# Performance work log

Measured on AMD Instinct MI355X. Metric: run time of the kernel, lower is better.

## Reference

```python
import jax, jax.numpy as jnp
import numpy as np

BN_EPS = 1e-3  # keras BatchNormalization default epsilon


def setup_inputs() -> dict:
    key = jax.random.key(0)
    ks = jax.random.split(key, 8)
    B, F, Df = 256, 64, 256   # batch, num_features, feature_dim
    E, H, D = 8, 256, 256     # num_experts, hidden, expert_dim
    s1 = 1.0 / np.sqrt(Df)
    s2 = 1.0 / np.sqrt(H)
    return {
        "x":  jax.random.normal(ks[0], (B, F, Df), jnp.float32),
        "Wr": jax.random.normal(ks[1], (Df, E), jnp.float32) * s1,
        "br": jnp.zeros((E,), jnp.float32),
        "W1": jax.random.normal(ks[2], (E, Df, H), jnp.float32) * s1,
        "b1": jnp.zeros((E, H), jnp.float32),
        "g1": jnp.ones((E, H), jnp.float32),
        "be1": jnp.zeros((E, H), jnp.float32),
        "m1": jnp.zeros((E, H), jnp.float32),
        "v1": jnp.ones((E, H), jnp.float32),
        "W2": jax.random.normal(ks[3], (E, H, H), jnp.float32) * s2,
        "b2": jnp.zeros((E, H), jnp.float32),
        "g2": jnp.ones((E, H), jnp.float32),
        "be2": jnp.zeros((E, H), jnp.float32),
        "m2": jnp.zeros((E, H), jnp.float32),
        "v2": jnp.ones((E, H), jnp.float32),
        "Wo": jax.random.normal(ks[4], (E, H, D), jnp.float32) * s2,
        "bo": jnp.zeros((E, D), jnp.float32),
    }


def _bn(h, g, b, m, v):
    # inference-mode batch norm with moving stats; params are [E,H], h is [B,F,E,H]
    return g * (h - m) * jax.lax.rsqrt(v + BN_EPS) + b


def reference(x, Wr, br, W1, b1, g1, be1, m1, v1,
              W2, b2, g2, be2, m2, v2, Wo, bo):
    # learned softmax routing: mean over batch -> [F, Df] -> dense -> softmax
    feat = jnp.mean(x, axis=0)                     # [F, Df]
    w = jax.nn.softmax(feat @ Wr + br, axis=-1)    # [F, E]

    # all experts at once: Dense -> BN -> relu, x2, then Dense output
    h = jnp.einsum('bfd,edh->bfeh', x, W1) + b1    # [B, F, E, H]
    h = jax.nn.relu(_bn(h, g1, be1, m1, v1))
    h = jnp.einsum('bfeh,ehk->bfek', h, W2) + b2
    h = jax.nn.relu(_bn(h, g2, be2, m2, v2))
    y = jnp.einsum('bfeh,ehd->bfed', h, Wo) + bo   # [B, F, E, D]

    # weighted combine over experts (routing weights broadcast over batch)
    return jnp.einsum('bfed,fe->bfd', y, w)        # [B, F, D]
```

## Files before the change

### kernel.cpp

```cpp
#include <hip/hip_runtime.h>
#include <hip/hip_bf16.h>
#include <stdint.h>

#define BN_EPS 1e-3f

typedef __bf16 bf16x8 __attribute__((ext_vector_type(8)));
typedef float  f32x16 __attribute__((ext_vector_type(16)));

static constexpr size_t WS_FOLD_OFF = 24ull * 131072ull;
static constexpr size_t WS_WRT_OFF  = WS_FOLD_OFF + 32768ull;
static constexpr size_t WS_WB_OFF   = WS_WRT_OFF + 2048ull;

#define XADDR(fr, tok) (((fr) << 10) + ((((tok) ^ (fr))) << 4))

__global__ __launch_bounds__(256) void fold_kernel(
    const float* __restrict__ b1, const float* __restrict__ g1, const float* __restrict__ be1,
    const float* __restrict__ m1, const float* __restrict__ v1,
    const float* __restrict__ b2, const float* __restrict__ g2, const float* __restrict__ be2,
    const float* __restrict__ m2, const float* __restrict__ v2,
    float* __restrict__ fold) {
  int i = blockIdx.x * 256 + threadIdx.x;
  if (i < 2048) {
    float s1 = g1[i] * rsqrtf(v1[i] + BN_EPS);
    fold[i]        = s1;
    fold[2048 + i] = (b1[i] - m1[i]) * s1 + be1[i];
    float s2 = g2[i] * rsqrtf(v2[i] + BN_EPS);
    fold[4096 + i] = s2;
    fold[6144 + i] = (b2[i] - m2[i]) * s2 + be2[i];
  }
}

__global__ __launch_bounds__(256) void pack_kernel(
    const float* __restrict__ W1, const float* __restrict__ W2, const float* __restrict__ Wo,
    __bf16* __restrict__ pk) {
  __shared__ float sl[16 * 256];
  int bid = blockIdx.x;
  int m = bid >> 4, ks = bid & 15;
  int L = m >> 3, e = m & 7;
  const float* Ws = (L == 0 ? W1 : (L == 1 ? W2 : Wo)) + (size_t)e * 65536 + (size_t)ks * 16 * 256;
  int t = threadIdx.x;
#pragma unroll
  for (int it = 0; it < 4; ++it) {
    int el4 = it * 256 + t;
    float4 v = *reinterpret_cast<const float4*>(Ws + (size_t)el4 * 4);
    *reinterpret_cast<float4*>(&sl[el4 * 4]) = v;
  }
  __syncthreads();
#pragma unroll
  for (int it = 0; it < 2; ++it) {
    int task = it * 256 + t;
    int nb = task >> 6, l = task & 63;
    int colb = nb * 32 + (l & 31);
    int krow = (l >> 5) * 8;
    union { __bf16 h[8]; int4 v; } u;
#pragma unroll
    for (int i = 0; i < 8; ++i) u.h[i] = (__bf16)sl[(krow + i) * 256 + colb];
    size_t off = ((size_t)(m * 8 + nb) * 16 + ks) * 512 + (size_t)l * 8;
    *reinterpret_cast<int4*>(pk + off) = u.v;
  }
}

__global__ __launch_bounds__(256) void route1_kernel(
    const float* __restrict__ x, float* __restrict__ part) {
  int f = blockIdx.x, bq = blockIdx.y, t = threadIdx.x;
  const float* xp = x + (size_t)(bq * 32) * 16384 + f * 256 + t;
  float s = 0.f;
#pragma unroll 4
  for (int bi = 0; bi < 32; ++bi) s += xp[(size_t)bi * 16384];
  part[(size_t)(bq * 64 + f) * 256 + t] = s;
}

__global__ __launch_bounds__(256) void route2_kernel(
    const float* __restrict__ part, const float* __restrict__ Wr, const float* __restrict__ br,
    const float* __restrict__ bo, float* __restrict__ wrt, float* __restrict__ wb) {
  __shared__ float feat[256];
  __shared__ float lg[8];
  __shared__ float wsm[8];
  int f = blockIdx.x, t = threadIdx.x;
  float a = 0.f;
#pragma unroll
  for (int bq = 0; bq < 8; ++bq) a += part[(size_t)(bq * 64 + f) * 256 + t];
  feat[t] = a * (1.0f / 256.0f);
  __syncthreads();
  if (t < 8) {
    float s = br[t];
    for (int d = 0; d < 256; ++d) s += feat[d] * Wr[d * 8 + t];
    lg[t] = s;
  }
  __syncthreads();
  if (t == 0) {
    float mx = lg[0];
#pragma unroll
    for (int e = 1; e < 8; ++e) mx = fmaxf(mx, lg[e]);
    float ex[8]; float sum = 0.f;
#pragma unroll
    for (int e = 0; e < 8; ++e) { ex[e] = expf(lg[e] - mx); sum += ex[e]; }
    float inv = 1.0f / sum;
#pragma unroll
    for (int e = 0; e < 8; ++e) { float v = ex[e] * inv; wsm[e] = v; wrt[f * 8 + e] = v; }
  }
  __syncthreads();
  float o = 0.f;
#pragma unroll
  for (int e = 0; e < 8; ++e) o += wsm[e] * bo[e * 256 + t];
  wb[f * 256 + t] = o;
}

__device__ __forceinline__ void sweep(
    const char* __restrict__ src, const __bf16* __restrict__ pb,
    int l, int l31, int hi, int swap, int zero, f32x16 acc[2]) {
  if (zero) {
#pragma unroll
    for (int mt = 0; mt < 2; ++mt)
#pragma unroll
      for (int r = 0; r < 16; ++r) acc[mt][r] = 0.f;
  }
  bf16x8 b0 = *reinterpret_cast<const bf16x8*>(pb + (size_t)l * 8);
  bf16x8 b1 = *reinterpret_cast<const bf16x8*>(pb + 512 + (size_t)l * 8);
#pragma unroll
  for (int ks = 0; ks < 16; ++ks) {
    bf16x8 bn = (ks < 14) ? *reinterpret_cast<const bf16x8*>(pb + (size_t)(ks + 2) * 512 + (size_t)l * 8) : b0;
    int fr = 2 * ks + hi;
    bf16x8 a0 = *reinterpret_cast<const bf16x8*>(src + XADDR(fr, l31));
    bf16x8 a1 = *reinterpret_cast<const bf16x8*>(src + XADDR(fr, 32 + l31));
    if (swap) {
      acc[0] = __builtin_amdgcn_mfma_f32_32x32x16_bf16(b0, a0, acc[0], 0, 0, 0);
      acc[1] = __builtin_amdgcn_mfma_f32_32x32x16_bf16(b0, a1, acc[1], 0, 0, 0);
    } else {
      acc[0] = __builtin_amdgcn_mfma_f32_32x32x16_bf16(a0, b0, acc[0], 0, 0, 0);
      acc[1] = __builtin_amdgcn_mfma_f32_32x32x16_bf16(a1, b0, acc[1], 0, 0, 0);
    }
    b0 = b1; b1 = bn;
  }
}

__device__ __forceinline__ void epi_store(
    const f32x16 acc[2], const float* __restrict__ sA, const float* __restrict__ cA,
    char* __restrict__ dst, int l31, int hi, int w, float w0, float w1) {
#pragma unroll
  for (int g = 0; g < 4; ++g) {
    float4 s4 = *reinterpret_cast<const float4*>(sA + 8 * g);
    float4 c4 = *reinterpret_cast<const float4*>(cA + 8 * g);
    int fr = w * 4 + g;
#pragma unroll
    for (int mt = 0; mt < 2; ++mt) {
      float wm = (mt == 0) ? w0 : w1;
      union { __bf16 h[4]; uint2 u; } p;
#pragma unroll
      for (int j = 0; j < 4; ++j) {
        float sj = (&s4.x)[j], cj = (&c4.x)[j];
        p.h[j] = (__bf16)(wm * fmaxf(acc[mt][4 * g + j] * sj + cj, 0.f));
      }
      *reinterpret_cast<uint2*>(dst + XADDR(fr, mt * 32 + l31) + hi * 8) = p.u;
    }
  }
}

__global__ __launch_bounds__(512, 4) void moe_kernel(
    const float* __restrict__ x, const __bf16* __restrict__ pk,
    const float* __restrict__ fold, const float* __restrict__ wrt,
    const float* __restrict__ wb, float* __restrict__ out) {
  __shared__ char xb[32768];
  __shared__ char hb[32768];
  __shared__ float wrts[512];
  const int tid = threadIdx.x;
  const int l = tid & 63, w = tid >> 6;
  const int l31 = l & 31, hi = l >> 5;
  const int bid = blockIdx.x;
  const int tile = bid >> 1, eh = bid & 1;

  {
    const float* xg = x + (size_t)tile * 16384;
#pragma unroll
    for (int i = 0; i < 4; ++i) {
      int u = i * 512 + tid;
      int tok = u >> 5, k8 = u & 31;
      const float* src = xg + (size_t)tok * 256 + k8 * 8;
      float4 v0 = *reinterpret_cast<const float4*>(src);
      float4 v1 = *reinterpret_cast<const float4*>(src + 4);
      union { __bf16 h[8]; int4 v; } p;
      p.h[0] = (__bf16)v0.x; p.h[1] = (__bf16)v0.y; p.h[2] = (__bf16)v0.z; p.h[3] = (__bf16)v0.w;
      p.h[4] = (__bf16)v1.x; p.h[5] = (__bf16)v1.y; p.h[6] = (__bf16)v1.z; p.h[7] = (__bf16)v1.w;
      *reinterpret_cast<int4*>(xb + XADDR(k8, tok)) = p.v;
    }
  }
  wrts[tid] = wrt[tid];

  f32x16 outacc[2];
#pragma unroll
  for (int mt = 0; mt < 2; ++mt)
#pragma unroll
    for (int r = 0; r < 16; ++r) outacc[mt][r] = 0.f;

  __syncthreads();

  f32x16 acc[2];
#pragma unroll 1
  for (int ep = 0; ep < 4; ++ep) {
    const int e = eh * 4 + ep;
    sweep(xb, pk + (size_t)((0 * 8 + e) * 8 + w) * 8192, l, l31, hi, 1, 1, acc);
    __syncthreads();
    epi_store(acc, fold + 0 * 4096 + e * 256 + w * 32 + 4 * hi,
              fold + 0 * 4096 + 2048 + e * 256 + w * 32 + 4 * hi, hb, l31, hi, w, 1.f, 1.f);
    __syncthreads();
    sweep(hb, pk + (size_t)((1 * 8 + e) * 8 + w) * 8192, l, l31, hi, 1, 1, acc);
    __syncthreads();
    {
      float w0 = wrts[l31 * 8 + e];
      float w1 = wrts[(32 + l31) * 8 + e];
      epi_store(acc, fold + 1 * 4096 + e * 256 + w * 32 + 4 * hi,
                fold + 1 * 4096 + 2048 + e * 256 + w * 32 + 4 * hi, hb, l31, hi, w, w0, w1);
    }
    __syncthreads();
    sweep(hb, pk + (size_t)((2 * 8 + e) * 8 + w) * 8192, l, l31, hi, 0, 0, outacc);
  }

  float* og = out + (size_t)tile * 16384;
  const int col = w * 32 + l31;
#pragma unroll
  for (int mt = 0; mt < 2; ++mt) {
#pragma unroll
    for (int r = 0; r < 16; ++r) {
      int row = mt * 32 + 4 * hi + (r & 3) + 8 * (r >> 2);
      float v = outacc[mt][r];
      if (eh == 0) v += wb[row * 256 + col];
      unsafeAtomicAdd(og + row * 256 + col, v);
    }
  }
}

extern "C" void kernel_launch(void* const* d_in, const int* in_sizes, int n_in,
                              void* d_out, int out_size, void* d_ws, size_t ws_size,
                              hipStream_t stream) {
  const float* x   = (const float*)d_in[0];
  const float* Wr  = (const float*)d_in[1];
  const float* br  = (const float*)d_in[2];
  const float* W1  = (const float*)d_in[3];
  const float* b1  = (const float*)d_in[4];
  const float* g1  = (const float*)d_in[5];
  const float* be1 = (const float*)d_in[6];
  const float* m1  = (const float*)d_in[7];
  const float* v1  = (const float*)d_in[8];
  const float* W2  = (const float*)d_in[9];
  const float* b2  = (const float*)d_in[10];
  const float* g2  = (const float*)d_in[11];
  const float* be2 = (const float*)d_in[12];
  const float* m2  = (const float*)d_in[13];
  const float* v2  = (const float*)d_in[14];
  const float* Wo  = (const float*)d_in[15];
  const float* bo  = (const float*)d_in[16];
  float* out = (float*)d_out;

  __bf16* pk  = (__bf16*)d_ws;
  float* part = (float*)d_ws;
  float* fold = (float*)((char*)d_ws + WS_FOLD_OFF);
  float* wrt  = (float*)((char*)d_ws + WS_WRT_OFF);
  float* wb   = (float*)((char*)d_ws + WS_WB_OFF);

  hipMemsetAsync(out, 0, (size_t)out_size * sizeof(float), stream);
  hipLaunchKernelGGL(route1_kernel, dim3(64, 8), dim3(256), 0, stream, x, part);
  hipLaunchKernelGGL(route2_kernel, dim3(64), dim3(256), 0, stream, part, Wr, br, bo, wrt, wb);
  hipLaunchKernelGGL(fold_kernel, dim3(8), dim3(256), 0, stream,
                     b1, g1, be1, m1, v1, b2, g2, be2, m2, v2, fold);
  hipLaunchKernelGGL(pack_kernel, dim3(384), dim3(256), 0, stream, W1, W2, Wo, pk);
  hipLaunchKernelGGL(moe_kernel, dim3(512), dim3(512), 0, stream, x, pk, fold, wrt, wb, out);
}
```

Baseline: 123.8 us.

## Enlarge MoE block tile to 128 tokens with 2x2 warp MFMA tiling

```diff
diff --git a/kernel.cpp b/kernel.cpp
--- a/kernel.cpp
+++ b/kernel.cpp
@@ -11,7 +11,7 @@
 static constexpr size_t WS_WRT_OFF  = WS_FOLD_OFF + 32768ull;
 static constexpr size_t WS_WB_OFF   = WS_WRT_OFF + 2048ull;
 
-#define XADDR(fr, tok) (((fr) << 10) + ((((tok) ^ (fr))) << 4))
+#define XADDR(fr, tok) (((fr) << 11) + ((((tok) ^ ((fr) & 31))) << 4))
 
 __global__ __launch_bounds__(256) void fold_kernel(
     const float* __restrict__ b1, const float* __restrict__ g1, const float* __restrict__ be1,
@@ -106,73 +106,82 @@
   wb[f * 256 + t] = o;
 }
 
-__device__ __forceinline__ void sweep(
+__device__ __forceinline__ void sweep128(
     const char* __restrict__ src, const __bf16* __restrict__ pb,
-    int l, int l31, int hi, int swap, int zero, f32x16 acc[2]) {
+    int l, int l31, int hi, int mtg, int swap, int zero, f32x16 acc[2][2]) {
   if (zero) {
 #pragma unroll
-    for (int mt = 0; mt < 2; ++mt)
-#pragma unroll
-      for (int r = 0; r < 16; ++r) acc[mt][r] = 0.f;
-  }
-  bf16x8 b0 = *reinterpret_cast<const bf16x8*>(pb + (size_t)l * 8);
-  bf16x8 b1 = *reinterpret_cast<const bf16x8*>(pb + 512 + (size_t)l * 8);
+    for (int nbi = 0; nbi < 2; ++nbi)
+#pragma unroll
+      for (int mt = 0; mt < 2; ++mt)
+#pragma unroll
+        for (int r = 0; r < 16; ++r) acc[nbi][mt][r] = 0.f;
+  }
 #pragma unroll
   for (int ks = 0; ks < 16; ++ks) {
-    bf16x8 bn = (ks < 14) ? *reinterpret_cast<const bf16x8*>(pb + (size_t)(ks + 2) * 512 + (size_t)l * 8) : b0;
+    bf16x8 b0 = *reinterpret_cast<const bf16x8*>(pb + (size_t)ks * 512 + (size_t)l * 8);
+    bf16x8 b1 = *reinterpret_cast<const bf16x8*>(pb + 8192 + (size_t)ks * 512 + (size_t)l * 8);
     int fr = 2 * ks + hi;
-    bf16x8 a0 = *reinterpret_cast<const bf16x8*>(src + XADDR(fr, l31));
-    bf16x8 a1 = *reinterpret_cast<const bf16x8*>(src + XADDR(fr, 32 + l31));
+    bf16x8 a0 = *reinterpret_cast<const bf16x8*>(src + XADDR(fr, mtg * 64 + l31));
+    bf16x8 a1 = *reinterpret_cast<const bf16x8*>(src + XADDR(fr, mtg * 64 + 32 + l31));
     if (swap) {
-      acc[0] = __builtin_amdgcn_mfma_f32_32x32x16_bf16(b0, a0, acc[0], 0, 0, 0);
-      acc[1] = __builtin_amdgcn_mfma_f32_32x32x16_bf16(b0, a1, acc[1], 0, 0, 0);
+      acc[0][0] = __builtin_amdgcn_mfma_f32_32x32x16_bf16(b0, a0, acc[0][0], 0, 0, 0);
+      acc[0][1] = __builtin_amdgcn_mfma_f32_32x32x16_bf16(b0, a1, acc[0][1], 0, 0, 0);
+      acc[1][0] = __builtin_amdgcn_mfma_f32_32x32x16_bf16(b1, a0, acc[1][0], 0, 0, 0);
+      acc[1][1] = __builtin_amdgcn_mfma_f32_32x32x16_bf16(b1, a1, acc[1][1], 0, 0, 0);
     } else {
-      acc[0] = __builtin_amdgcn_mfma_f32_32x32x16_bf16(a0, b0, acc[0], 0, 0, 0);
-      acc[1] = __builtin_amdgcn_mfma_f32_32x32x16_bf16(a1, b0, acc[1], 0, 0, 0);
-    }
-    b0 = b1; b1 = bn;
+      acc[0][0] = __builtin_amdgcn_mfma_f32_32x32x16_bf16(a0, b0, acc[0][0], 0, 0, 0);
+      acc[0][1] = __builtin_amdgcn_mfma_f32_32x32x16_bf16(a1, b0, acc[0][1], 0, 0, 0);
+      acc[1][0] = __builtin_amdgcn_mfma_f32_32x32x16_bf16(a0, b1, acc[1][0], 0, 0, 0);
+      acc[1][1] = __builtin_amdgcn_mfma_f32_32x32x16_bf16(a1, b1, acc[1][1], 0, 0, 0);
+    }
   }
 }
 
 __device__ __forceinline__ void epi_store(
-    const f32x16 acc[2], const float* __restrict__ sA, const float* __restrict__ cA,
-    char* __restrict__ dst, int l31, int hi, int w, float w0, float w1) {
-#pragma unroll
-  for (int g = 0; g < 4; ++g) {
-    float4 s4 = *reinterpret_cast<const float4*>(sA + 8 * g);
-    float4 c4 = *reinterpret_cast<const float4*>(cA + 8 * g);
-    int fr = w * 4 + g;
-#pragma unroll
-    for (int mt = 0; mt < 2; ++mt) {
-      float wm = (mt == 0) ? w0 : w1;
-      union { __bf16 h[4]; uint2 u; } p;
-#pragma unroll
-      for (int j = 0; j < 4; ++j) {
-        float sj = (&s4.x)[j], cj = (&c4.x)[j];
-        p.h[j] = (__bf16)(wm * fmaxf(acc[mt][4 * g + j] * sj + cj, 0.f));
+    const f32x16 acc[2][2], const float* __restrict__ sA, const float* __restrict__ cA,
+    char* __restrict__ dst, int l31, int hi, int mtg, int wn, float w0, float w1) {
+#pragma unroll
+  for (int nbi = 0; nbi < 2; ++nbi) {
+#pragma unroll
+    for (int g = 0; g < 4; ++g) {
+      float4 s4 = *reinterpret_cast<const float4*>(sA + nbi * 32 + 8 * g);
+      float4 c4 = *reinterpret_cast<const float4*>(cA + nbi * 32 + 8 * g);
+      int fr = (wn * 2 + nbi) * 4 + g;
+#pragma unroll
+      for (int mt = 0; mt < 2; ++mt) {
+        float wm = (mt == 0) ? w0 : w1;
+        union { __bf16 h[4]; uint2 u; } p;
+#pragma unroll
+        for (int j = 0; j < 4; ++j) {
+          float sj = (&s4.x)[j], cj = (&c4.x)[j];
+          p.h[j] = (__bf16)(wm * fmaxf(acc[nbi][mt][4 * g + j] * sj + cj, 0.f));
+        }
+        int tok = mtg * 64 + mt * 32 + l31;
+        *reinterpret_cast<uint2*>(dst + XADDR(fr, tok) + hi * 8) = p.u;
       }
-      *reinterpret_cast<uint2*>(dst + XADDR(fr, mt * 32 + l31) + hi * 8) = p.u;
-    }
-  }
-}
-
-__global__ __launch_bounds__(512, 4) void moe_kernel(
+    }
+  }
+}
+
+__global__ __launch_bounds__(512, 2) void moe_kernel(
     const float* __restrict__ x, const __bf16* __restrict__ pk,
     const float* __restrict__ fold, const float* __restrict__ wrt,
     const float* __restrict__ wb, float* __restrict__ out) {
-  __shared__ char xb[32768];
-  __shared__ char hb[32768];
+  __shared__ char xb[65536];
+  __shared__ char hb[65536];
   __shared__ float wrts[512];
   const int tid = threadIdx.x;
   const int l = tid & 63, w = tid >> 6;
   const int l31 = l & 31, hi = l >> 5;
+  const int wn = w & 3, mtg = w >> 2;
   const int bid = blockIdx.x;
   const int tile = bid >> 1, eh = bid & 1;
 
   {
-    const float* xg = x + (size_t)tile * 16384;
-#pragma unroll
-    for (int i = 0; i < 4; ++i) {
+    const float* xg = x + (size_t)tile * 32768;
+#pragma unroll
+    for (int i = 0; i < 8; ++i) {
       int u = i * 512 + tid;
       int tok = u >> 5, k8 = u & 31;
       const float* src = xg + (size_t)tok * 256 + k8 * 8;
@@ -186,45 +195,51 @@
   }
   wrts[tid] = wrt[tid];
 
-  f32x16 outacc[2];
-#pragma unroll
-  for (int mt = 0; mt < 2; ++mt)
-#pragma unroll
-    for (int r = 0; r < 16; ++r) outacc[mt][r] = 0.f;
-
-  __syncthreads();
-
-  f32x16 acc[2];
+  f32x16 outacc[2][2];
+#pragma unroll
+  for (int nbi = 0; nbi < 2; ++nbi)
+#pragma unroll
+    for (int mt = 0; mt < 2; ++mt)
+#pragma unroll
+      for (int r = 0; r < 16; ++r) outacc[nbi][mt][r] = 0.f;
+
+  __syncthreads();
+
+  f32x16 acc[2][2];
 #pragma unroll 1
   for (int ep = 0; ep < 4; ++ep) {
     const int e = eh * 4 + ep;
-    sweep(xb, pk + (size_t)((0 * 8 + e) * 8 + w) * 8192, l, l31, hi, 1, 1, acc);
-    __syncthreads();
-    epi_store(acc, fold + 0 * 4096 + e * 256 + w * 32 + 4 * hi,
-              fold + 0 * 4096 + 2048 + e * 256 + w * 32 + 4 * hi, hb, l31, hi, w, 1.f, 1.f);
-    __syncthreads();
-    sweep(hb, pk + (size_t)((1 * 8 + e) * 8 + w) * 8192, l, l31, hi, 1, 1, acc);
+    sweep128(xb, pk + (size_t)((0 * 8 + e) * 8 + wn * 2) * 8192, l, l31, hi, mtg, 1, 1, acc);
+    __syncthreads();
+    epi_store(acc, fold + 0 * 4096 + e * 256 + wn * 64 + 4 * hi,
+              fold + 0 * 4096 + 2048 + e * 256 + wn * 64 + 4 * hi, hb, l31, hi, mtg, wn, 1.f, 1.f);
+    __syncthreads();
+    sweep128(hb, pk + (size_t)((1 * 8 + e) * 8 + wn * 2) * 8192, l, l31, hi, mtg, 1, 1, acc);
     __syncthreads();
     {
       float w0 = wrts[l31 * 8 + e];
       float w1 = wrts[(32 + l31) * 8 + e];
-      epi_store(acc, fold + 1 * 4096 + e * 256 + w * 32 + 4 * hi,
-                fold + 1 * 4096 + 2048 + e * 256 + w * 32 + 4 * hi, hb, l31, hi, w, w0, w1);
-    }
-    __syncthreads();
-    sweep(hb, pk + (size_t)((2 * 8 + e) * 8 + w) * 8192, l, l31, hi, 0, 0, outacc);
-  }
-
-  float* og = out + (size_t)tile * 16384;
-  const int col = w * 32 + l31;
-#pragma unroll
-  for (int mt = 0; mt < 2; ++mt) {
-#pragma unroll
-    for (int r = 0; r < 16; ++r) {
-      int row = mt * 32 + 4 * hi + (r & 3) + 8 * (r >> 2);
-      float v = outacc[mt][r];
-      if (eh == 0) v += wb[row * 256 + col];
-      unsafeAtomicAdd(og + row * 256 + col, v);
+      epi_store(acc, fold + 1 * 4096 + e * 256 + wn * 64 + 4 * hi,
+                fold + 1 * 4096 + 2048 + e * 256 + wn * 64 + 4 * hi, hb, l31, hi, mtg, wn, w0, w1);
+    }
+    __syncthreads();
+    sweep128(hb, pk + (size_t)((2 * 8 + e) * 8 + wn * 2) * 8192, l, l31, hi, mtg, 0, 0, outacc);
+  }
+
+  float* og = out + (size_t)tile * 32768;
+#pragma unroll
+  for (int nbi = 0; nbi < 2; ++nbi) {
+    int col = (wn * 2 + nbi) * 32 + l31;
+#pragma unroll
+    for (int mt = 0; mt < 2; ++mt) {
+#pragma unroll
+      for (int r = 0; r < 16; ++r) {
+        int f = mt * 32 + 4 * hi + (r & 3) + 8 * (r >> 2);
+        int row = mtg * 64 + f;
+        float v = outacc[nbi][mt][r];
+        if (eh == 0) v += wb[f * 256 + col];
+        unsafeAtomicAdd(og + row * 256 + col, v);
+      }
     }
   }
 }
@@ -263,5 +278,5 @@
   hipLaunchKernelGGL(fold_kernel, dim3(8), dim3(256), 0, stream,
                      b1, g1, be1, m1, v1, b2, g2, be2, m2, v2, fold);
   hipLaunchKernelGGL(pack_kernel, dim3(384), dim3(256), 0, stream, W1, W2, Wo, pk);
-  hipLaunchKernelGGL(moe_kernel, dim3(512), dim3(512), 0, stream, x, pk, fold, wrt, wb, out);
-}
+  hipLaunchKernelGGL(moe_kernel, dim3(256), dim3(512), 0, stream, x, pk, fold, wrt, wb, out);
+}
```

Result: slower. 137.5 us (+11.0%).

## Pipeline MFMA sweeps with cross-layer weight prefetch and merge setup kernels

Applied to the files above, without the earlier changes.

```diff
diff --git a/kernel.cpp b/kernel.cpp
--- a/kernel.cpp
+++ b/kernel.cpp
@@ -7,20 +7,32 @@
 typedef __bf16 bf16x8 __attribute__((ext_vector_type(8)));
 typedef float  f32x16 __attribute__((ext_vector_type(16)));
 
+#define MFMA __builtin_amdgcn_mfma_f32_32x32x16_bf16
+
 static constexpr size_t WS_FOLD_OFF = 24ull * 131072ull;
 static constexpr size_t WS_WRT_OFF  = WS_FOLD_OFF + 32768ull;
 static constexpr size_t WS_WB_OFF   = WS_WRT_OFF + 2048ull;
 
-#define XADDR(fr, tok) (((fr) << 10) + ((((tok) ^ (fr))) << 4))
-
-__global__ __launch_bounds__(256) void fold_kernel(
+#define XADDR64(fr, tok) (((fr) << 10) + ((((tok) ^ ((fr) & 31))) << 4))
+
+#define LBAR() do { \
+  asm volatile("s_waitcnt lgkmcnt(0)" ::: "memory"); \
+  __builtin_amdgcn_s_barrier(); \
+  asm volatile("" ::: "memory"); \
+} while (0)
+
+__global__ __launch_bounds__(256) void pack_kernel(
+    const float* __restrict__ W1, const float* __restrict__ W2, const float* __restrict__ Wo,
     const float* __restrict__ b1, const float* __restrict__ g1, const float* __restrict__ be1,
     const float* __restrict__ m1, const float* __restrict__ v1,
     const float* __restrict__ b2, const float* __restrict__ g2, const float* __restrict__ be2,
     const float* __restrict__ m2, const float* __restrict__ v2,
-    float* __restrict__ fold) {
-  int i = blockIdx.x * 256 + threadIdx.x;
-  if (i < 2048) {
+    __bf16* __restrict__ pk, float* __restrict__ fold) {
+  __shared__ float sl[16 * 256];
+  int bid = blockIdx.x;
+  int t = threadIdx.x;
+  if (bid < 8) {
+    int i = bid * 256 + t;
     float s1 = g1[i] * rsqrtf(v1[i] + BN_EPS);
     fold[i]        = s1;
     fold[2048 + i] = (b1[i] - m1[i]) * s1 + be1[i];
@@ -28,17 +40,9 @@
     fold[4096 + i] = s2;
     fold[6144 + i] = (b2[i] - m2[i]) * s2 + be2[i];
   }
-}
-
-__global__ __launch_bounds__(256) void pack_kernel(
-    const float* __restrict__ W1, const float* __restrict__ W2, const float* __restrict__ Wo,
-    __bf16* __restrict__ pk) {
-  __shared__ float sl[16 * 256];
-  int bid = blockIdx.x;
   int m = bid >> 4, ks = bid & 15;
   int L = m >> 3, e = m & 7;
   const float* Ws = (L == 0 ? W1 : (L == 1 ? W2 : Wo)) + (size_t)e * 65536 + (size_t)ks * 16 * 256;
-  int t = threadIdx.x;
 #pragma unroll
   for (int it = 0; it < 4; ++it) {
     int el4 = it * 256 + t;
@@ -61,8 +65,14 @@
 }
 
 __global__ __launch_bounds__(256) void route1_kernel(
-    const float* __restrict__ x, float* __restrict__ part) {
-  int f = blockIdx.x, bq = blockIdx.y, t = threadIdx.x;
+    const float* __restrict__ x, float* __restrict__ part, float* __restrict__ out) {
+  int g = blockIdx.x;
+  int f = g & 63, bq = g >> 6;
+  int t = threadIdx.x;
+  float4 z = {0.f, 0.f, 0.f, 0.f};
+  float4* oz = reinterpret_cast<float4*>(out + (size_t)g * 8192);
+#pragma unroll
+  for (int i = 0; i < 8; ++i) oz[i * 256 + t] = z;
   const float* xp = x + (size_t)(bq * 32) * 16384 + f * 256 + t;
   float s = 0.f;
 #pragma unroll 4
@@ -106,53 +116,60 @@
   wb[f * 256 + t] = o;
 }
 
-__device__ __forceinline__ void sweep(
+template<int SWAP, int ZERO>
+__device__ __forceinline__ void sweep64(
     const char* __restrict__ src, const __bf16* __restrict__ pb,
-    int l, int l31, int hi, int swap, int zero, f32x16 acc[2]) {
-  if (zero) {
-#pragma unroll
-    for (int mt = 0; mt < 2; ++mt)
-#pragma unroll
-      for (int r = 0; r < 16; ++r) acc[mt][r] = 0.f;
-  }
-  bf16x8 b0 = *reinterpret_cast<const bf16x8*>(pb + (size_t)l * 8);
-  bf16x8 b1 = *reinterpret_cast<const bf16x8*>(pb + 512 + (size_t)l * 8);
-#pragma unroll
-  for (int ks = 0; ks < 16; ++ks) {
-    bf16x8 bn = (ks < 14) ? *reinterpret_cast<const bf16x8*>(pb + (size_t)(ks + 2) * 512 + (size_t)l * 8) : b0;
-    int fr = 2 * ks + hi;
-    bf16x8 a0 = *reinterpret_cast<const bf16x8*>(src + XADDR(fr, l31));
-    bf16x8 a1 = *reinterpret_cast<const bf16x8*>(src + XADDR(fr, 32 + l31));
-    if (swap) {
-      acc[0] = __builtin_amdgcn_mfma_f32_32x32x16_bf16(b0, a0, acc[0], 0, 0, 0);
-      acc[1] = __builtin_amdgcn_mfma_f32_32x32x16_bf16(b0, a1, acc[1], 0, 0, 0);
-    } else {
-      acc[0] = __builtin_amdgcn_mfma_f32_32x32x16_bf16(a0, b0, acc[0], 0, 0, 0);
-      acc[1] = __builtin_amdgcn_mfma_f32_32x32x16_bf16(a1, b0, acc[1], 0, 0, 0);
-    }
-    b0 = b1; b1 = bn;
-  }
-}
-
-__device__ __forceinline__ void epi_store(
-    const f32x16 acc[2], const float* __restrict__ sA, const float* __restrict__ cA,
-    char* __restrict__ dst, int l31, int hi, int w, float w0, float w1) {
+    const __bf16* __restrict__ pbn, int l, int l31, int hi,
+    bf16x8& c0, bf16x8& c1, bf16x8& c2, bf16x8& c3,
+    f32x16& accA, f32x16& accB) {
+  if (ZERO) {
+#pragma unroll
+    for (int r = 0; r < 16; ++r) { accA[r] = 0.f; accB[r] = 0.f; }
+  }
+  bf16x8 a0 = *reinterpret_cast<const bf16x8*>(src + XADDR64(hi, l31));
+  bf16x8 a1 = *reinterpret_cast<const bf16x8*>(src + XADDR64(hi, 32 + l31));
+
+#define SW_STEP(KS, CV)                                                              \
+  {                                                                                  \
+    bf16x8 na0, na1;                                                                 \
+    if ((KS) < 15) {                                                                 \
+      na0 = *reinterpret_cast<const bf16x8*>(src + XADDR64(2 * ((KS) + 1) + hi, l31));        \
+      na1 = *reinterpret_cast<const bf16x8*>(src + XADDR64(2 * ((KS) + 1) + hi, 32 + l31));   \
+    }                                                                                \
+    __builtin_amdgcn_s_setprio(1);                                                   \
+    if (SWAP) { accA = MFMA(CV, a0, accA, 0, 0, 0); accB = MFMA(CV, a1, accB, 0, 0, 0); } \
+    else      { accA = MFMA(a0, CV, accA, 0, 0, 0); accB = MFMA(a1, CV, accB, 0, 0, 0); } \
+    __builtin_amdgcn_s_setprio(0);                                                   \
+    CV = *reinterpret_cast<const bf16x8*>(                                           \
+        (((KS) < 12) ? (pb + ((KS) + 4) * 512) : (pbn + ((KS) - 12) * 512)) + (size_t)l * 8); \
+    if ((KS) < 15) { a0 = na0; a1 = na1; }                                           \
+  }
+
+  SW_STEP(0, c0)  SW_STEP(1, c1)  SW_STEP(2, c2)  SW_STEP(3, c3)
+  SW_STEP(4, c0)  SW_STEP(5, c1)  SW_STEP(6, c2)  SW_STEP(7, c3)
+  SW_STEP(8, c0)  SW_STEP(9, c1)  SW_STEP(10, c2) SW_STEP(11, c3)
+  SW_STEP(12, c0) SW_STEP(13, c1) SW_STEP(14, c2) SW_STEP(15, c3)
+#undef SW_STEP
+}
+
+__device__ __forceinline__ void epi64(
+    const f32x16& accA, const f32x16& accB,
+    const float* __restrict__ sA, const float* __restrict__ cA,
+    char* __restrict__ dst, int l31, int hi, int wn, float w0, float w1) {
 #pragma unroll
   for (int g = 0; g < 4; ++g) {
     float4 s4 = *reinterpret_cast<const float4*>(sA + 8 * g);
     float4 c4 = *reinterpret_cast<const float4*>(cA + 8 * g);
-    int fr = w * 4 + g;
-#pragma unroll
-    for (int mt = 0; mt < 2; ++mt) {
-      float wm = (mt == 0) ? w0 : w1;
-      union { __bf16 h[4]; uint2 u; } p;
-#pragma unroll
-      for (int j = 0; j < 4; ++j) {
-        float sj = (&s4.x)[j], cj = (&c4.x)[j];
-        p.h[j] = (__bf16)(wm * fmaxf(acc[mt][4 * g + j] * sj + cj, 0.f));
-      }
-      *reinterpret_cast<uint2*>(dst + XADDR(fr, mt * 32 + l31) + hi * 8) = p.u;
+    int fr = wn * 4 + g;
+    union { __bf16 h[4]; uint2 u; } pA, pB;
+#pragma unroll
+    for (int j = 0; j < 4; ++j) {
+      float sj = (&s4.x)[j], cj = (&c4.x)[j];
+      pA.h[j] = (__bf16)(w0 * fmaxf(accA[4 * g + j] * sj + cj, 0.f));
+      pB.h[j] = (__bf16)(w1 * fmaxf(accB[4 * g + j] * sj + cj, 0.f));
     }
+    *reinterpret_cast<uint2*>(dst + XADDR64(fr, l31) + hi * 8) = pA.u;
+    *reinterpret_cast<uint2*>(dst + XADDR64(fr, 32 + l31) + hi * 8) = pB.u;
   }
 }
 
@@ -164,10 +181,19 @@
   __shared__ char hb[32768];
   __shared__ float wrts[512];
   const int tid = threadIdx.x;
-  const int l = tid & 63, w = tid >> 6;
+  const int l = tid & 63;
   const int l31 = l & 31, hi = l >> 5;
+  const int wn = __builtin_amdgcn_readfirstlane(tid >> 6);
   const int bid = blockIdx.x;
-  const int tile = bid >> 1, eh = bid & 1;
+  const int tile = bid & 255, eh = bid >> 8;
+
+#define PBO(L, e) (pk + (size_t)((((L) * 8 + (e)) * 8 + wn) * 8192))
+
+  const __bf16* pbf = PBO(0, eh * 4);
+  bf16x8 rc0 = *reinterpret_cast<const bf16x8*>(pbf + 0 * 512 + (size_t)l * 8);
+  bf16x8 rc1 = *reinterpret_cast<const bf16x8*>(pbf + 1 * 512 + (size_t)l * 8);
+  bf16x8 rc2 = *reinterpret_cast<const bf16x8*>(pbf + 2 * 512 + (size_t)l * 8);
+  bf16x8 rc3 = *reinterpret_cast<const bf16x8*>(pbf + 3 * 512 + (size_t)l * 8);
 
   {
     const float* xg = x + (size_t)tile * 16384;
@@ -181,51 +207,55 @@
       union { __bf16 h[8]; int4 v; } p;
       p.h[0] = (__bf16)v0.x; p.h[1] = (__bf16)v0.y; p.h[2] = (__bf16)v0.z; p.h[3] = (__bf16)v0.w;
       p.h[4] = (__bf16)v1.x; p.h[5] = (__bf16)v1.y; p.h[6] = (__bf16)v1.z; p.h[7] = (__bf16)v1.w;
-      *reinterpret_cast<int4*>(xb + XADDR(k8, tok)) = p.v;
+      *reinterpret_cast<int4*>(xb + XADDR64(k8, tok)) = p.v;
     }
   }
   wrts[tid] = wrt[tid];
 
-  f32x16 outacc[2];
-#pragma unroll
-  for (int mt = 0; mt < 2; ++mt)
-#pragma unroll
-    for (int r = 0; r < 16; ++r) outacc[mt][r] = 0.f;
-
-  __syncthreads();
-
-  f32x16 acc[2];
+  f32x16 outA, outB;
+#pragma unroll
+  for (int r = 0; r < 16; ++r) { outA[r] = 0.f; outB[r] = 0.f; }
+
+  LBAR();
+
+  f32x16 accA, accB;
 #pragma unroll 1
   for (int ep = 0; ep < 4; ++ep) {
     const int e = eh * 4 + ep;
-    sweep(xb, pk + (size_t)((0 * 8 + e) * 8 + w) * 8192, l, l31, hi, 1, 1, acc);
-    __syncthreads();
-    epi_store(acc, fold + 0 * 4096 + e * 256 + w * 32 + 4 * hi,
-              fold + 0 * 4096 + 2048 + e * 256 + w * 32 + 4 * hi, hb, l31, hi, w, 1.f, 1.f);
-    __syncthreads();
-    sweep(hb, pk + (size_t)((1 * 8 + e) * 8 + w) * 8192, l, l31, hi, 1, 1, acc);
-    __syncthreads();
+    const __bf16* pb_l0 = PBO(0, e);
+    const __bf16* pb_l1 = PBO(1, e);
+    const __bf16* pb_l2 = PBO(2, e);
+    const __bf16* pb_nx = (ep < 3) ? PBO(0, e + 1) : PBO(0, eh * 4);
+    sweep64<1, 1>(xb, pb_l0, pb_l1, l, l31, hi, rc0, rc1, rc2, rc3, accA, accB);
+    LBAR();
+    epi64(accA, accB, fold + e * 256 + wn * 32 + 4 * hi,
+          fold + 2048 + e * 256 + wn * 32 + 4 * hi, hb, l31, hi, wn, 1.f, 1.f);
+    LBAR();
+    sweep64<1, 1>(hb, pb_l1, pb_l2, l, l31, hi, rc0, rc1, rc2, rc3, accA, accB);
+    LBAR();
     {
       float w0 = wrts[l31 * 8 + e];
       float w1 = wrts[(32 + l31) * 8 + e];
-      epi_store(acc, fold + 1 * 4096 + e * 256 + w * 32 + 4 * hi,
-                fold + 1 * 4096 + 2048 + e * 256 + w * 32 + 4 * hi, hb, l31, hi, w, w0, w1);
+      epi64(accA, accB, fold + 4096 + e * 256 + wn * 32 + 4 * hi,
+            fold + 6144 + e * 256 + wn * 32 + 4 * hi, hb, l31, hi, wn, w0, w1);
     }
-    __syncthreads();
-    sweep(hb, pk + (size_t)((2 * 8 + e) * 8 + w) * 8192, l, l31, hi, 0, 0, outacc);
-  }
+    LBAR();
+    sweep64<0, 0>(hb, pb_l2, pb_nx, l, l31, hi, rc0, rc1, rc2, rc3, outA, outB);
+  }
+#undef PBO
 
   float* og = out + (size_t)tile * 16384;
-  const int col = w * 32 + l31;
-#pragma unroll
-  for (int mt = 0; mt < 2; ++mt) {
-#pragma unroll
-    for (int r = 0; r < 16; ++r) {
-      int row = mt * 32 + 4 * hi + (r & 3) + 8 * (r >> 2);
-      float v = outacc[mt][r];
-      if (eh == 0) v += wb[row * 256 + col];
-      unsafeAtomicAdd(og + row * 256 + col, v);
-    }
+  const int col = wn * 32 + l31;
+#pragma unroll
+  for (int r = 0; r < 16; ++r) {
+    int fA = 4 * hi + (r & 3) + 8 * (r >> 2);
+    float vA = outA[r];
+    if (eh == 0) vA += wb[fA * 256 + col];
+    unsafeAtomicAdd(og + fA * 256 + col, vA);
+    int fB = 32 + fA;
+    float vB = outB[r];
+    if (eh == 0) vB += wb[fB * 256 + col];
+    unsafeAtomicAdd(og + fB * 256 + col, vB);
   }
 }
 
@@ -257,11 +287,9 @@
   float* wrt  = (float*)((char*)d_ws + WS_WRT_OFF);
   float* wb   = (float*)((char*)d_ws + WS_WB_OFF);
 
-  hipMemsetAsync(out, 0, (size_t)out_size * sizeof(float), stream);
-  hipLaunchKernelGGL(route1_kernel, dim3(64, 8), dim3(256), 0, stream, x, part);
+  hipLaunchKernelGGL(route1_kernel, dim3(512), dim3(256), 0, stream, x, part, out);
   hipLaunchKernelGGL(route2_kernel, dim3(64), dim3(256), 0, stream, part, Wr, br, bo, wrt, wb);
-  hipLaunchKernelGGL(fold_kernel, dim3(8), dim3(256), 0, stream,
-                     b1, g1, be1, m1, v1, b2, g2, be2, m2, v2, fold);
-  hipLaunchKernelGGL(pack_kernel, dim3(384), dim3(256), 0, stream, W1, W2, Wo, pk);
+  hipLaunchKernelGGL(pack_kernel, dim3(384), dim3(256), 0, stream,
+                     W1, W2, Wo, b1, g1, be1, m1, v1, b2, g2, be2, m2, v2, pk, fold);
   hipLaunchKernelGGL(moe_kernel, dim3(512), dim3(512), 0, stream, x, pk, fold, wrt, wb, out);
 }
```

Result: slower. 149.1 us (+20.4%).
